# Kernel tuning notes

Hardware: AMD Instinct MI355X
Metric: run time of the kernel (lower is better)

The kernel has to match this reference:

```python
import jax, jax.numpy as jnp
import numpy as np

N, F, H, O = 16384, 64, 128, 512

def setup_inputs() -> dict:
    key = jax.random.key(0)
    ks = jax.random.split(key, 5)
    # PyTorch Linear default init: U(-1/sqrt(fan_in), 1/sqrt(fan_in))
    lim1 = 1.0  # fan_in = 1 for Linear(1, H)
    lim2 = 1.0 / np.sqrt(H)
    x = jax.random.normal(ks[0], (N, F), dtype=jnp.float32)
    W1 = jax.random.uniform(ks[1], (F, H), minval=-lim1, maxval=lim1, dtype=jnp.float32)
    b1 = jax.random.uniform(ks[2], (F, H), minval=-lim1, maxval=lim1, dtype=jnp.float32)
    W2 = jax.random.uniform(ks[3], (F, H, O), minval=-lim2, maxval=lim2, dtype=jnp.float32)
    b2 = jax.random.uniform(ks[4], (F, O), minval=-lim2, maxval=lim2, dtype=jnp.float32)
    return {"x": x, "W1": W1, "b1": b1, "W2": W2, "b2": b2}

def reference(x, W1, b1, W2, b2):
    # Per-feature MLP: h_f = W2_f @ elu(x_f * w1_f + b1_f) + b2_f, summed over f.
    # pre: [N, F, H] = outer-product of each scalar feature with its W1 row
    pre = x[:, :, None] * W1[None, :, :] + b1[None, :, :]
    a = jax.nn.elu(pre)                                  # [N, F, H]
    h = jnp.einsum('nfh,fho->no', a, W2)                 # sum over f and h
    h = h + jnp.sum(b2, axis=0)[None, :]                 # biases summed over F
    return h / jnp.sqrt(jnp.float32(F))
```

## Files before the change

### kernel.cpp

```cpp
#include <hip/hip_runtime.h>
#include <cstdint>

#define NROWS 16384
#define FDIM 64
#define HDIM 128
#define ODIM 512
#define KDIM 8192

#define BM 64
#define BN 512
#define BK 64
#define NST 128

typedef short bf16x8 __attribute__((ext_vector_type(8)));
typedef float f32x4 __attribute__((ext_vector_type(4)));
typedef uint32_t u32x4 __attribute__((ext_vector_type(4)));

__device__ __forceinline__ uint16_t rne_bf16(float f) {
  uint32_t u = __builtin_bit_cast(uint32_t, f);
  u += 0x7fffu + ((u >> 16) & 1u);
  return (uint16_t)(u >> 16);
}

__global__ void prep_w2f(const float* __restrict__ W2, uint16_t* __restrict__ W2F,
                         const float* __restrict__ b2, float* __restrict__ b2sum) {
  __shared__ float tile[64][65];
  const int k0 = blockIdx.x * 64;
  const int o0 = blockIdx.y * 64;
  const int tx = threadIdx.x;
  const int ty = threadIdx.y;
#pragma unroll
  for (int j = 0; j < 8; ++j)
    tile[ty + 8 * j][tx] = W2[(size_t)(k0 + ty + 8 * j) * ODIM + o0 + tx];
  __syncthreads();
  const int o = o0 + tx;
  u32x4 ov;
#pragma unroll
  for (int p = 0; p < 4; ++p) {
    const uint32_t lo = rne_bf16(tile[ty * 8 + 2 * p][tx]);
    const uint32_t hi = rne_bf16(tile[ty * 8 + 2 * p + 1][tx]);
    ov[p] = lo | (hi << 16);
  }
  const size_t idx = (size_t)(o >> 4) * 131072 + (size_t)((k0 >> 5) + (ty >> 2)) * 512 +
                     (size_t)(((o & 15) + 16 * (ty & 3)) * 8);
  *(u32x4*)&W2F[idx] = ov;

  if (blockIdx.x == 0 && blockIdx.y == 0) {
    const int t = ty * 64 + tx;
    float s = 0.f;
#pragma unroll
    for (int f = 0; f < FDIM; ++f) s += b2[(size_t)f * ODIM + t];
    b2sum[t] = s;
  }
}

struct Pref {
  f32x4 wlo, whi, blo, bhi;
  float xv;
};

__global__ __launch_bounds__(512, 2) void mlp_gemm(
    const float* __restrict__ x, const float* __restrict__ W1,
    const float* __restrict__ b1, const uint16_t* __restrict__ W2F,
    const float* __restrict__ b2sum, float* __restrict__ out) {
  __shared__ __align__(16) uint16_t As0[BM * BK];
  __shared__ __align__(16) uint16_t As1[BM * BK];

  const int tid = threadIdx.x;
  const int m0 = blockIdx.x * BM;

  const int wid = tid >> 6;
  const int lane = tid & 63;
  const int wn = wid * 64;
  const int q = lane >> 4;
  const int r = lane & 15;

  const int ar = tid >> 3;
  const int ac = tid & 7;
  const int awc = (ac ^ (ar & 7)) * 8;

  const uint16_t* wbase = W2F + (size_t)(wid * 4) * 131072 + (size_t)lane * 8;

  f32x4 acc[4][4];
#pragma unroll
  for (int i = 0; i < 4; ++i)
#pragma unroll
    for (int j = 0; j < 4; ++j) acc[i][j] = {0.f, 0.f, 0.f, 0.f};

  auto ldops = [&](Pref& P, int s) {
    const int f = s >> 1;
    const int hoff = (s & 1) * 64 + ac * 8;
    const float* wp = W1 + (size_t)f * HDIM + hoff;
    const float* bp = b1 + (size_t)f * HDIM + hoff;
    P.wlo = *(const f32x4*)wp;
    P.whi = *(const f32x4*)(wp + 4);
    P.blo = *(const f32x4*)bp;
    P.bhi = *(const f32x4*)(bp + 4);
    P.xv = x[(size_t)(m0 + ar) * FDIM + f];
  };

  auto ldB = [&](bf16x8* Bf, int kk) {
#pragma unroll
    for (int kc = 0; kc < 2; ++kc)
#pragma unroll
      for (int nt = 0; nt < 4; ++nt)
        Bf[kc * 4 + nt] =
            *(const bf16x8*)(wbase + ((size_t)nt * 256 + kk * 2 + kc) * 512);
  };

  auto eluA = [&](uint16_t* Ab, const Pref& P) {
    u32x4 ov;
#pragma unroll
    for (int p = 0; p < 4; ++p) {
      const float we0 = (p < 2) ? P.wlo[2 * p] : P.whi[2 * p - 4];
      const float we1 = (p < 2) ? P.wlo[2 * p + 1] : P.whi[2 * p - 3];
      const float be0 = (p < 2) ? P.blo[2 * p] : P.bhi[2 * p - 4];
      const float be1 = (p < 2) ? P.blo[2 * p + 1] : P.bhi[2 * p - 3];
      float plo = fmaf(P.xv, we0, be0);
      float phi = fmaf(P.xv, we1, be1);
      float elo = plo > 0.f ? plo : __expf(plo) - 1.f;
      float ehi = phi > 0.f ? phi : __expf(phi) - 1.f;
      ov[p] = __builtin_amdgcn_perm(__builtin_bit_cast(uint32_t, ehi),
                                    __builtin_bit_cast(uint32_t, elo),
                                    0x07060302u);
    }
    *(u32x4*)&Ab[ar * BK + awc] = ov;
  };

  auto compute = [&](const uint16_t* Ab, const bf16x8* Bf) {
#pragma unroll
    for (int kc = 0; kc < 2; ++kc) {
      bf16x8 af[4];
      const int cg = kc * 4 + q;
#pragma unroll
      for (int mt = 0; mt < 4; ++mt) {
        const int row = mt * 16 + r;
        af[mt] = *(const bf16x8*)&Ab[row * BK + ((cg ^ (row & 7)) * 8)];
      }
#pragma unroll
      for (int mt = 0; mt < 4; ++mt)
#pragma unroll
        for (int nt = 0; nt < 4; ++nt)
          acc[mt][nt] = __builtin_amdgcn_mfma_f32_16x16x32_bf16(
              af[mt], Bf[kc * 4 + nt], acc[mt][nt], 0, 0, 0);
    }
  };

  Pref Pa, Pb;
  bf16x8 Bf0[8], Bf1[8];

  ldops(Pa, 0);
  eluA(As0, Pa);
  ldops(Pa, 1);
  __syncthreads();

#pragma unroll 1
  for (int kk = 0; kk < NST - 2; kk += 2) {
    ldB(Bf0, kk);
    ldops(Pb, kk + 2);
    __builtin_amdgcn_sched_barrier(0);
    eluA(As1, Pa);
    compute(As0, Bf0);
    __syncthreads();
    ldB(Bf1, kk + 1);
    ldops(Pa, kk + 3);
    __builtin_amdgcn_sched_barrier(0);
    eluA(As0, Pb);
    compute(As1, Bf1);
    __syncthreads();
  }
  ldB(Bf0, NST - 2);
  __builtin_amdgcn_sched_barrier(0);
  eluA(As1, Pa);
  compute(As0, Bf0);
  __syncthreads();
  ldB(Bf1, NST - 1);
  compute(As1, Bf1);

  float bsv[4];
#pragma unroll
  for (int nt = 0; nt < 4; ++nt) bsv[nt] = b2sum[wn + nt * 16 + r];
#pragma unroll
  for (int mt = 0; mt < 4; ++mt)
#pragma unroll
    for (int nt = 0; nt < 4; ++nt)
#pragma unroll
      for (int v = 0; v < 4; ++v) {
        const int row = m0 + mt * 16 + q * 4 + v;
        const int col = wn + nt * 16 + r;
        out[(size_t)row * ODIM + col] = (acc[mt][nt][v] + bsv[nt]) * 0.125f;
      }
}

extern "C" void kernel_launch(void* const* d_in, const int* in_sizes, int n_in,
                              void* d_out, int out_size, void* d_ws, size_t ws_size,
                              hipStream_t stream) {
  const float* x  = (const float*)d_in[0];
  const float* W1 = (const float*)d_in[1];
  const float* b1 = (const float*)d_in[2];
  const float* W2 = (const float*)d_in[3];
  const float* b2 = (const float*)d_in[4];
  float* out = (float*)d_out;

  char* ws = (char*)d_ws;
  float*    b2sum = (float*)ws;
  uint16_t* W2F   = (uint16_t*)(ws + 65536);

  prep_w2f<<<dim3(KDIM / 64, ODIM / 64), dim3(64, 8), 0, stream>>>(W2, W2F, b2, b2sum);
  mlp_gemm<<<NROWS / BM, 512, 0, stream>>>(x, W1, b1, W2F, b2sum, out);
}
```

Baseline: 246.7 us.

## Interleave W2 layout by K-step and prefetch B fragments one stage ahead

Reorders the packed bf16 W2 layout so that all output tiles for a given K-step sit next to each other in memory, which lets the eight waves of a block read one contiguous region per stage. Register prefetch of B fragments moves one stage earlier, so each stage's global loads overlap the previous stage's MFMAs. It also reduces the operand prefetch registers to a single set and loads A fragments per row tile inside the MFMA loop, aiming to lower register pressure. The risks are a longer B-load lifetime that raises VGPR use, and possible stalls if the compiler cannot hide the LDS reads that now sit next to the MFMAs.

```diff
diff --git a/kernel.cpp b/kernel.cpp
--- a/kernel.cpp
+++ b/kernel.cpp
@@ -41,8 +41,9 @@
     const uint32_t hi = rne_bf16(tile[ty * 8 + 2 * p + 1][tx]);
     ov[p] = lo | (hi << 16);
   }
-  const size_t idx = (size_t)(o >> 4) * 131072 + (size_t)((k0 >> 5) + (ty >> 2)) * 512 +
-                     (size_t)(((o & 15) + 16 * (ty & 3)) * 8);
+  const size_t idx =
+      ((size_t)((k0 >> 5) + (ty >> 2)) * 32 + (o >> 4)) * 512 +
+      (size_t)(((o & 15) + 16 * (ty & 3)) * 8);
   *(u32x4*)&W2F[idx] = ov;
 
   if (blockIdx.x == 0 && blockIdx.y == 0) {
@@ -79,7 +80,7 @@
   const int ac = tid & 7;
   const int awc = (ac ^ (ar & 7)) * 8;
 
-  const uint16_t* wbase = W2F + (size_t)(wid * 4) * 131072 + (size_t)lane * 8;
+  const uint16_t* wbase = W2F + (size_t)lane * 8;
 
   f32x4 acc[4][4];
 #pragma unroll
@@ -104,8 +105,8 @@
     for (int kc = 0; kc < 2; ++kc)
 #pragma unroll
       for (int nt = 0; nt < 4; ++nt)
-        Bf[kc * 4 + nt] =
-            *(const bf16x8*)(wbase + ((size_t)nt * 256 + kk * 2 + kc) * 512);
+        Bf[kc * 4 + nt] = *(const bf16x8*)(
+            wbase + ((size_t)(kk * 2 + kc) * 32 + wid * 4 + nt) * 512);
   };
 
   auto eluA = [&](uint16_t* Ab, const Pref& P) {
@@ -130,52 +131,49 @@
   auto compute = [&](const uint16_t* Ab, const bf16x8* Bf) {
 #pragma unroll
     for (int kc = 0; kc < 2; ++kc) {
-      bf16x8 af[4];
       const int cg = kc * 4 + q;
 #pragma unroll
       for (int mt = 0; mt < 4; ++mt) {
         const int row = mt * 16 + r;
-        af[mt] = *(const bf16x8*)&Ab[row * BK + ((cg ^ (row & 7)) * 8)];
-      }
-#pragma unroll
-      for (int mt = 0; mt < 4; ++mt)
+        const bf16x8 af = *(const bf16x8*)&Ab[row * BK + ((cg ^ (row & 7)) * 8)];
 #pragma unroll
         for (int nt = 0; nt < 4; ++nt)
           acc[mt][nt] = __builtin_amdgcn_mfma_f32_16x16x32_bf16(
-              af[mt], Bf[kc * 4 + nt], acc[mt][nt], 0, 0, 0);
+              af, Bf[kc * 4 + nt], acc[mt][nt], 0, 0, 0);
+      }
     }
   };
 
-  Pref Pa, Pb;
-  bf16x8 Bf0[8], Bf1[8];
-
-  ldops(Pa, 0);
-  eluA(As0, Pa);
-  ldops(Pa, 1);
+  Pref P;
+  bf16x8 B0[8], B1[8];
+
+  ldops(P, 0);
+  ldB(B0, 0);
+  eluA(As0, P);
+  ldops(P, 1);
   __syncthreads();
 
 #pragma unroll 1
   for (int kk = 0; kk < NST - 2; kk += 2) {
-    ldB(Bf0, kk);
-    ldops(Pb, kk + 2);
+    eluA(As1, P);
+    ldB(B1, kk + 1);
+    ldops(P, kk + 2);
     __builtin_amdgcn_sched_barrier(0);
-    eluA(As1, Pa);
-    compute(As0, Bf0);
+    compute(As0, B0);
     __syncthreads();
-    ldB(Bf1, kk + 1);
-    ldops(Pa, kk + 3);
+    eluA(As0, P);
+    ldB(B0, kk + 2);
+    ldops(P, kk + 3);
     __builtin_amdgcn_sched_barrier(0);
-    eluA(As0, Pb);
-    compute(As1, Bf1);
+    compute(As1, B1);
     __syncthreads();
   }
-  ldB(Bf0, NST - 2);
+  eluA(As1, P);
+  ldB(B1, NST - 1);
   __builtin_amdgcn_sched_barrier(0);
-  eluA(As1, Pa);
-  compute(As0, Bf0);
+  compute(As0, B0);
   __syncthreads();
-  ldB(Bf1, NST - 1);
-  compute(As1, Bf1);
+  compute(As1, B1);
 
   float bsv[4];
 #pragma unroll
```

Result: faster. 232.6 us (-5.7%).
